# Performance work log

Measured on AMD Instinct MI355X. Metric: run time of the kernel, lower is better.

The kernel has to match this reference:

```python
import jax, jax.numpy as jnp
import numpy as np

B, T, S, H = 32, 512, 1024, 512


def setup_inputs() -> dict:
    key = jax.random.key(0)
    k1, k2, k3, k4, k5, k6 = jax.random.split(key, 6)
    scale = 1.0 / np.sqrt(H)
    return {
        "query": jax.random.normal(k1, (B, T, H), dtype=jnp.float32),
        "encoder_outputs": jax.random.normal(k2, (B, S, H), dtype=jnp.float32),
        "src_lengths": jax.random.randint(k3, (B,), 1, S + 1, dtype=jnp.int32),
        "Ws": jax.random.normal(k4, (H, H), dtype=jnp.float32) * scale,  # torch Linear weight [out,in]
        "Wh": jax.random.normal(k5, (H, H), dtype=jnp.float32) * scale,
        "v": jax.random.normal(k6, (H,), dtype=jnp.float32) * scale,
    }


def reference(query, encoder_outputs, src_lengths, Ws, Wh, v):
    # score(h_s, q_t) = v^T tanh(Wh h_s + Ws q_t); masked softmax over src; weighted sum.
    S_ = encoder_outputs.shape[1]
    # Wh(encoder_outputs) computed once (loop in original recomputes it each step; same math).
    Whe = jnp.einsum('bsh,oh->bso', encoder_outputs, Wh)  # [B,S,H]
    mask = jnp.arange(S_)[None, :] < src_lengths[:, None]  # [B,S] valid positions

    def step(carry, q_t):  # q_t: [B,H]
        Wsq = jnp.einsum('bh,oh->bo', q_t, Ws)            # [B,H]
        scores = jnp.einsum('bsh,h->bs', jnp.tanh(Whe + Wsq[:, None, :]), v)  # [B,S]
        scores = jnp.where(mask, scores, -jnp.inf)
        attn = jax.nn.softmax(scores, axis=-1)            # [B,S]
        ctx = jnp.einsum('bs,bsh->bh', attn, encoder_outputs)  # [B,H]
        return carry, (ctx, attn)

    _, (ctx_t, attn_t) = jax.lax.scan(step, None, jnp.swapaxes(query, 0, 1))
    context_vectors = jnp.swapaxes(ctx_t, 0, 1)  # [B,T,H]
    # original returns attention weights from the LAST timestep only
    return context_vectors, attn_t[-1]
```

## Files before the change

### kernel.cpp

```cpp
#include <hip/hip_runtime.h>


constexpr int B = 32, T = 512, S = 1024, H = 512;
constexpr int TT = 16;
constexpr float C2LOG2E = 2.88539008177792681f;

typedef float vf4 __attribute__((ext_vector_type(4)));
typedef float f32x4 __attribute__((ext_vector_type(4)));
typedef short bf16x8 __attribute__((ext_vector_type(8)));
typedef unsigned short ushort_t;

#define DEVI __device__ __forceinline__

DEVI unsigned pack_bf16(float a, float b) {
  unsigned ua = __builtin_bit_cast(unsigned, a) + 0x8000u;
  unsigned ub = __builtin_bit_cast(unsigned, b) + 0x8000u;
  return (ub & 0xffff0000u) | (ua >> 16);
}
DEVI ushort_t to_bf16u(float x) {
  return (ushort_t)((__builtin_bit_cast(unsigned, x) + 0x8000u) >> 16);
}
DEVI float bf_lo(unsigned d) { return __builtin_bit_cast(float, d << 16); }
DEVI float bf_hi(unsigned d) { return __builtin_bit_cast(float, d & 0xffff0000u); }
DEVI float bf_one(ushort_t u) { return __builtin_bit_cast(float, (unsigned)u << 16); }
DEVI float exp2c(float x) {
  return __builtin_amdgcn_exp2f(fminf(fmaxf(x, -15.f), 15.f));
}

constexpr int QBLK = (B * T / 128) * 4;
constexpr int EBLK = (B * S / 128) * 4;

__global__ __launch_bounds__(256)
void mfma_matmul_kernel(const float* __restrict__ query, const float* __restrict__ enc,
                        const float* __restrict__ Ws, const float* __restrict__ Wh,
                        float* __restrict__ q4, float* __restrict__ e4,
                        const int* __restrict__ lens) {
  __shared__ short As[128][72];
  __shared__ short Bs[128][72];
  const int tid = threadIdx.x;
  int blk = blockIdx.x;
  const bool isE = blk >= QBLK;
  if (isE) blk -= QBLK;
  const int bx = blk & 3, by = blk >> 2;
  const int row0 = by * 128, col0 = bx * 128;
  const float* A = isE ? enc : query;
  const float* W = isE ? Wh : Ws;
  if (isE && (row0 % S) >= lens[row0 / S]) return;

  const int lr = tid >> 4;
  const int lc = (tid & 15) * 4;
  const int lane = tid & 63, wv = tid >> 6;
  const int wm = (wv >> 1) * 64, wn = (wv & 1) * 64;
  const int lrow = lane & 15, lkg = (lane >> 4) * 8;

  f32x4 acc[4][4] = {};
  for (int k0 = 0; k0 < H; k0 += 64) {
    __syncthreads();
#pragma unroll
    for (int u = 0; u < 8; ++u) {
      int r = lr + u * 16;
      float4 av = *(const float4*)&A[(size_t)(row0 + r) * H + k0 + lc];
      *(uint2*)&As[r][lc] = make_uint2(pack_bf16(av.x, av.y), pack_bf16(av.z, av.w));
      float4 wv4 = *(const float4*)&W[(size_t)(col0 + r) * H + k0 + lc];
      *(uint2*)&Bs[r][lc] = make_uint2(pack_bf16(wv4.x, wv4.y), pack_bf16(wv4.z, wv4.w));
    }
    __syncthreads();
#pragma unroll
    for (int ks = 0; ks < 64; ks += 32) {
      bf16x8 af[4], bfr[4];
#pragma unroll
      for (int i = 0; i < 4; ++i) {
        af[i] = *(const bf16x8*)&As[wm + i * 16 + lrow][ks + lkg];
        bfr[i] = *(const bf16x8*)&Bs[wn + i * 16 + lrow][ks + lkg];
      }
#pragma unroll
      for (int mt = 0; mt < 4; ++mt)
#pragma unroll
        for (int nt = 0; nt < 4; ++nt)
          acc[mt][nt] = __builtin_amdgcn_mfma_f32_16x16x32_bf16(
              af[mt], bfr[nt], acc[mt][nt], 0, 0, 0);
    }
  }

  const int crow = (lane >> 4) * 4, ccol = lane & 15;
  if (!isE) {
    const int b = row0 / T;
#pragma unroll
    for (int mt = 0; mt < 4; ++mt) {
      const int m = (row0 % T) + wm + mt * 16 + crow;
      const int tile_t = m >> 2;
#pragma unroll
      for (int nt = 0; nt < 4; ++nt) {
        const int n = col0 + wn + nt * 16 + ccol;
        float* base = q4 + (size_t)b * T * H + (size_t)tile_t * (4 * H) +
                      (n >> 2) * 16 + (n & 3);
        f32x4 a = acc[mt][nt];
#pragma unroll
        for (int reg = 0; reg < 4; ++reg) base[reg * 4] = exp2c(C2LOG2E * a[reg]);
      }
    }
  } else {
    const int b = row0 / S;
#pragma unroll
    for (int mt = 0; mt < 4; ++mt) {
      const int s0 = (row0 % S) + wm + mt * 16 + crow;
#pragma unroll
      for (int nt = 0; nt < 4; ++nt) {
        const int n = col0 + wn + nt * 16 + ccol;
        float* base = e4 + (size_t)b * H * S + (size_t)(n >> 2) * (4 * S) +
                      (size_t)s0 * 4 + (n & 3);
        f32x4 a = acc[mt][nt];
#pragma unroll
        for (int reg = 0; reg < 4; ++reg) base[reg * 4] = exp2c(C2LOG2E * a[reg]);
      }
    }
  }
}

DEVI void tree4(float& acc, vf4 q, vf4 vv, vf4 e) {
  float a0 = __builtin_fmaf(q[0], e[0], 1.0f);
  float a1 = __builtin_fmaf(q[1], e[1], 1.0f);
  float a2 = __builtin_fmaf(q[2], e[2], 1.0f);
  float a3 = __builtin_fmaf(q[3], e[3], 1.0f);
  float d01 = a0 * a1, d23 = a2 * a3;
  float n01 = __builtin_fmaf(vv[1], a0, vv[0] * a1);
  float n23 = __builtin_fmaf(vv[3], a2, vv[2] * a3);
  float d = d01 * d23;
  float n = __builtin_fmaf(n23, d01, n01 * d23);
  acc = __builtin_fmaf(n, __builtin_amdgcn_rcpf(d), acc);
}

DEVI vf4 qload4(const ushort_t (&s_q4)[32][64], int h4q, int t) {
  uint2 qu = *(const uint2*)&s_q4[h4q][t * 4];
  vf4 q = {bf_lo(qu.x), bf_hi(qu.x), bf_lo(qu.y), bf_hi(qu.y)};
  return q;
}

DEVI void stage_quarter(ushort_t (&s_q4)[32][64], const vf4* __restrict__ qsrc,
                        int qt, int tid) {
  __syncthreads();
#pragma unroll
  for (int u = 0; u < 2; ++u) {
    int g = tid + u * 256;
    int tile = g >> 7, rem = g & 127;
    int h4q = rem >> 2, i = rem & 3;
    vf4 qv = qsrc[tile * 512 + (qt * 32 + h4q) * 4 + i];
    uint2 pk = make_uint2(pack_bf16(qv[0], qv[1]), pack_bf16(qv[2], qv[3]));
    ((uint2*)&s_q4[0][0])[h4q * 16 + tile * 4 + i] = pk;
  }
  __syncthreads();
}

template <int NSIM>
DEVI void passN16(ushort_t (&s_q4)[32][64], const vf4* __restrict__ qsrc,
                  const float* __restrict__ v, const float* __restrict__ e4b,
                  ushort_t (&s_sc16)[TT][S], int wv, int lane) {
  const int tid = wv * 64 + lane;
  float acc[NSIM][TT];
#pragma unroll
  for (int r = 0; r < NSIM; ++r)
#pragma unroll
    for (int t = 0; t < TT; ++t) acc[r][t] = 0.f;
  const float* ep = e4b + (size_t)(wv * 64 + lane) * 4;
  for (int qt = 0; qt < 4; ++qt) {
    stage_quarter(s_q4, qsrc, qt, tid);
    for (int h4q = 0; h4q < 32; ++h4q) {
      const int h4 = qt * 32 + h4q;
      vf4 e[NSIM];
#pragma unroll
      for (int r = 0; r < NSIM; ++r)
        e[r] = *(const vf4*)(ep + (size_t)h4 * (S * 4) + r * 1024);
      vf4 vv = *(const vf4*)(v + h4 * 4);
#pragma unroll
      for (int t = 0; t < TT; ++t) {
        vf4 q = qload4(s_q4, h4q, t);
#pragma unroll
        for (int r = 0; r < NSIM; ++r) tree4(acc[r][t], q, vv, e[r]);
      }
    }
  }
#pragma unroll
  for (int r = 0; r < NSIM; ++r) {
    const int s = (wv + 4 * r) * 64 + lane;
#pragma unroll
    for (int t = 0; t < TT; ++t) s_sc16[t][s] = to_bf16u(-2.0f * acc[r][t]);
  }
}

template <int R>
DEVI void passTail16(ushort_t (&s_q4)[32][64], const vf4* __restrict__ qsrc,
                     const float* __restrict__ v, const float* __restrict__ e4b,
                     ushort_t (&s_sc16)[TT][S], int kbase, int wv, int lane) {
  const int tid = wv * 64 + lane;
  float acc[R][4];
#pragma unroll
  for (int r = 0; r < R; ++r)
#pragma unroll
    for (int jj = 0; jj < 4; ++jj) acc[r][jj] = 0.f;
  const float* ep = e4b + (size_t)(kbase * 64 + lane) * 4;
  for (int qt = 0; qt < 4; ++qt) {
    stage_quarter(s_q4, qsrc, qt, tid);
    for (int h4q = 0; h4q < 32; ++h4q) {
      const int h4 = qt * 32 + h4q;
      vf4 vv = *(const vf4*)(v + h4 * 4);
      vf4 e[R];
#pragma unroll
      for (int r = 0; r < R; ++r)
        e[r] = *(const vf4*)(ep + (size_t)h4 * (S * 4) + r * 256);
#pragma unroll
      for (int jj = 0; jj < 4; ++jj) {
        vf4 q = qload4(s_q4, h4q, wv + 4 * jj);
#pragma unroll
        for (int r = 0; r < R; ++r) tree4(acc[r][jj], q, vv, e[r]);
      }
    }
  }
#pragma unroll
  for (int r = 0; r < R; ++r)
#pragma unroll
    for (int jj = 0; jj < 4; ++jj)
      s_sc16[wv + 4 * jj][(kbase + r) * 64 + lane] = to_bf16u(-2.0f * acc[r][jj]);
}

__global__ __launch_bounds__(256, 4)
void attn_fused_kernel(const float* __restrict__ wsq, const float* __restrict__ wheT,
                       const float* __restrict__ enc, const float* __restrict__ v,
                       const int* __restrict__ lens, float* __restrict__ out) {
  __shared__ __align__(16) ushort_t s_sc16[TT][S];
  __shared__ __align__(16) ushort_t s_q4[32][64];
  __shared__ float s_rs[TT];
  __shared__ long long s_w[32];
  __shared__ int s_bsel;

  const int tid = threadIdx.x;
  const int xcd = blockIdx.x & 7;
  const int j = blockIdx.x >> 3;
  const int slot = j >> 5;
  const int tt = j & 31;

  if (tid < 32) s_w[tid] = ((long long)lens[tid] << 8) + tid;
  __syncthreads();
  if (tid < 32) {
    long long wb = s_w[tid];
    int rank = 0;
#pragma unroll
    for (int b2 = 0; b2 < 32; ++b2) rank += (s_w[b2] > wb);
    int myrank = slot * 8 + ((slot & 1) ? (7 - xcd) : xcd);
    if (rank == myrank) s_bsel = tid;
  }
  __syncthreads();
  const int b = __builtin_amdgcn_readfirstlane(s_bsel);
  const int len = lens[b];

  {
    const int wv = tid >> 6, lane = tid & 63;
    const int NS = (len + 63) >> 6;
    const int nsw = NS >> 2;
    const int R = NS & 3;
    const float* e4b = wheT + (size_t)b * H * S;
    const vf4* qsrc = (const vf4*)(wsq + (size_t)b * T * H + (size_t)tt * (TT * H));
    switch (nsw) {
      case 1: passN16<1>(s_q4, qsrc, v, e4b, s_sc16, wv, lane); break;
      case 2: passN16<2>(s_q4, qsrc, v, e4b, s_sc16, wv, lane); break;
      case 3: passN16<3>(s_q4, qsrc, v, e4b, s_sc16, wv, lane); break;
      case 4: passN16<4>(s_q4, qsrc, v, e4b, s_sc16, wv, lane); break;
      default: break;
    }
    switch (R) {
      case 1: passTail16<1>(s_q4, qsrc, v, e4b, s_sc16, nsw * 4, wv, lane); break;
      case 2: passTail16<2>(s_q4, qsrc, v, e4b, s_sc16, nsw * 4, wv, lane); break;
      case 3: passTail16<3>(s_q4, qsrc, v, e4b, s_sc16, nsw * 4, wv, lane); break;
      default: break;
    }
  }
  __syncthreads();

  {
    const int wv = tid >> 6, lane = tid & 63;
#pragma unroll
    for (int jj = 0; jj < 4; ++jj) {
      const int tr = wv + 4 * jj;
      float vals[S / 64], ps[S / 64];
      float m = -3.0e38f;
#pragma unroll
      for (int i = 0; i < S / 64; ++i) {
        int s = lane + 64 * i;
        vals[i] = bf_one(s_sc16[tr][s]);
        if (s < len) m = fmaxf(m, vals[i]);
      }
#pragma unroll
      for (int o = 1; o < 64; o <<= 1) m = fmaxf(m, __shfl_xor(m, o, 64));
      float sum = 0.f;
#pragma unroll
      for (int i = 0; i < S / 64; ++i) {
        int s = lane + 64 * i;
        float p = (s < len) ? __builtin_amdgcn_exp2f((vals[i] - m) * 1.44269504088896341f) : 0.f;
        ps[i] = p;
        sum += p;
      }
#pragma unroll
      for (int o = 1; o < 64; o <<= 1) sum += __shfl_xor(sum, o, 64);
      float rs = 1.0f / sum;
#pragma unroll
      for (int i = 0; i < S / 64; ++i) s_sc16[tr][lane + 64 * i] = to_bf16u(ps[i]);
      if (lane == 0) s_rs[tr] = rs;
      if (tt == T / TT - 1 && tr == TT - 1) {
#pragma unroll
        for (int i = 0; i < S / 64; ++i)
          out[(size_t)B * T * H + (size_t)b * S + lane + 64 * i] = ps[i] * rs;
      }
    }
  }
  __syncthreads();

  {
    const int wv = tid >> 6, lane = tid & 63;
    const int h0 = lane * 4, h1 = 256 + lane * 4;
    float acc[4][8] = {};
    const float* encb = enc + (size_t)b * S * H;
    const int len4 = (len + 3) & ~3;
    for (int s0 = 0; s0 < len4; s0 += 4) {
      vf4 pr[4];
#pragma unroll
      for (int jj = 0; jj < 4; ++jj) {
        uint2 pu = *(const uint2*)&s_sc16[wv + 4 * jj][s0];
        pr[jj] = (vf4){bf_lo(pu.x), bf_hi(pu.x), bf_lo(pu.y), bf_hi(pu.y)};
      }
#pragma unroll
      for (int kk = 0; kk < 4; ++kk) {
        const float* er = encb + (size_t)(s0 + kk) * H;
        float4 e0 = *(const float4*)(er + h0);
        float4 e1 = *(const float4*)(er + h1);
        float ev[8] = {e0.x, e0.y, e0.z, e0.w, e1.x, e1.y, e1.z, e1.w};
#pragma unroll
        for (int jj = 0; jj < 4; ++jj)
#pragma unroll
          for (int q = 0; q < 8; ++q)
            acc[jj][q] = __builtin_fmaf(pr[jj][kk], ev[q], acc[jj][q]);
      }
    }
#pragma unroll
    for (int jj = 0; jj < 4; ++jj) {
      const int tr = wv + 4 * jj;
      const float rs = s_rs[tr];
      const size_t base = ((size_t)b * T + tt * TT + tr) * H;
      float4 o;
      o = make_float4(acc[jj][0] * rs, acc[jj][1] * rs, acc[jj][2] * rs, acc[jj][3] * rs);
      *(float4*)&out[base + h0] = o;
      o = make_float4(acc[jj][4] * rs, acc[jj][5] * rs, acc[jj][6] * rs, acc[jj][7] * rs);
      *(float4*)&out[base + h1] = o;
    }
  }
}

extern "C" void kernel_launch(void* const* d_in, const int* in_sizes, int n_in,
                              void* d_out, int out_size, void* d_ws, size_t ws_size,
                              hipStream_t stream) {
  const float* query = (const float*)d_in[0];
  const float* enc   = (const float*)d_in[1];
  const int*   lens  = (const int*)d_in[2];
  const float* Ws    = (const float*)d_in[3];
  const float* Wh    = (const float*)d_in[4];
  const float* v     = (const float*)d_in[5];
  float* out = (float*)d_out;
  float* wsq  = (float*)d_ws;
  float* wheT = wsq + (size_t)B * T * H;

  mfma_matmul_kernel<<<dim3(QBLK + EBLK), 256, 0, stream>>>(query, enc, Ws, Wh, wsq, wheT, lens);
  attn_fused_kernel<<<dim3(B * (T / TT)), 256, 0, stream>>>(wsq, wheT, enc, v, lens, out);
}
```

Measured before the change: 560.5 us.

## Compute context accumulation with bf16 MFMA and drop softmax max pass

The context-vector stage is rewritten from per-thread scalar FMAs over float4 encoder rows to bf16 16x16x32 MFMA instructions. Attention probabilities are now taken straight from LDS, and encoder values are converted to bf16 on the fly. Softmax skips the max-reduction pass because tanh-bounded scores cannot overflow exp, and it normalizes probabilities before storing them. The score LDS buffer rows are padded to reduce bank conflicts. In exchange, encoder values lose precision in bf16, and the encoder loads become strided scalar reads instead of wide vector loads.

```diff
diff --git a/kernel.cpp b/kernel.cpp
--- a/kernel.cpp
+++ b/kernel.cpp
@@ -3,6 +3,7 @@
 
 constexpr int B = 32, T = 512, S = 1024, H = 512;
 constexpr int TT = 16;
+constexpr int SP = S + 8;
 constexpr float C2LOG2E = 2.88539008177792681f;
 
 typedef float vf4 __attribute__((ext_vector_type(4)));
@@ -154,7 +155,7 @@
 template <int NSIM>
 DEVI void passN16(ushort_t (&s_q4)[32][64], const vf4* __restrict__ qsrc,
                   const float* __restrict__ v, const float* __restrict__ e4b,
-                  ushort_t (&s_sc16)[TT][S], int wv, int lane) {
+                  ushort_t (&s_sc16)[TT][SP], int wv, int lane) {
   const int tid = wv * 64 + lane;
   float acc[NSIM][TT];
 #pragma unroll
@@ -190,7 +191,7 @@
 template <int R>
 DEVI void passTail16(ushort_t (&s_q4)[32][64], const vf4* __restrict__ qsrc,
                      const float* __restrict__ v, const float* __restrict__ e4b,
-                     ushort_t (&s_sc16)[TT][S], int kbase, int wv, int lane) {
+                     ushort_t (&s_sc16)[TT][SP], int kbase, int wv, int lane) {
   const int tid = wv * 64 + lane;
   float acc[R][4];
 #pragma unroll
@@ -226,9 +227,8 @@
 void attn_fused_kernel(const float* __restrict__ wsq, const float* __restrict__ wheT,
                        const float* __restrict__ enc, const float* __restrict__ v,
                        const int* __restrict__ lens, float* __restrict__ out) {
-  __shared__ __align__(16) ushort_t s_sc16[TT][S];
+  __shared__ __align__(16) ushort_t s_sc16[TT][SP];
   __shared__ __align__(16) ushort_t s_q4[32][64];
-  __shared__ float s_rs[TT];
   __shared__ long long s_w[32];
   __shared__ int s_bsel;
 
@@ -280,21 +280,13 @@
 #pragma unroll
     for (int jj = 0; jj < 4; ++jj) {
       const int tr = wv + 4 * jj;
-      float vals[S / 64], ps[S / 64];
-      float m = -3.0e38f;
+      float ps[S / 64];
+      float sum = 0.f;
 #pragma unroll
       for (int i = 0; i < S / 64; ++i) {
         int s = lane + 64 * i;
-        vals[i] = bf_one(s_sc16[tr][s]);
-        if (s < len) m = fmaxf(m, vals[i]);
-      }
-#pragma unroll
-      for (int o = 1; o < 64; o <<= 1) m = fmaxf(m, __shfl_xor(m, o, 64));
-      float sum = 0.f;
-#pragma unroll
-      for (int i = 0; i < S / 64; ++i) {
-        int s = lane + 64 * i;
-        float p = (s < len) ? __builtin_amdgcn_exp2f((vals[i] - m) * 1.44269504088896341f) : 0.f;
+        float sc = bf_one(s_sc16[tr][s]);
+        float p = (s < len) ? __builtin_amdgcn_exp2f(sc * 1.44269504088896341f) : 0.f;
         ps[i] = p;
         sum += p;
       }
@@ -302,12 +294,11 @@
       for (int o = 1; o < 64; o <<= 1) sum += __shfl_xor(sum, o, 64);
       float rs = 1.0f / sum;
 #pragma unroll
-      for (int i = 0; i < S / 64; ++i) s_sc16[tr][lane + 64 * i] = to_bf16u(ps[i]);
-      if (lane == 0) s_rs[tr] = rs;
-      if (tt == T / TT - 1 && tr == TT - 1) {
-#pragma unroll
-        for (int i = 0; i < S / 64; ++i)
-          out[(size_t)B * T * H + (size_t)b * S + lane + 64 * i] = ps[i] * rs;
+      for (int i = 0; i < S / 64; ++i) {
+        float pn = ps[i] * rs;
+        s_sc16[tr][lane + 64 * i] = to_bf16u(pn);
+        if (tt == T / TT - 1 && tr == TT - 1)
+          out[(size_t)B * T * H + (size_t)b * S + lane + 64 * i] = pn;
       }
     }
   }
@@ -315,40 +306,35 @@
 
   {
     const int wv = tid >> 6, lane = tid & 63;
-    const int h0 = lane * 4, h1 = 256 + lane * 4;
-    float acc[4][8] = {};
+    const int lrow = lane & 15, lkg = (lane >> 4) * 8;
+    const int hbase = wv * 128;
     const float* encb = enc + (size_t)b * S * H;
-    const int len4 = (len + 3) & ~3;
-    for (int s0 = 0; s0 < len4; s0 += 4) {
-      vf4 pr[4];
-#pragma unroll
-      for (int jj = 0; jj < 4; ++jj) {
-        uint2 pu = *(const uint2*)&s_sc16[wv + 4 * jj][s0];
-        pr[jj] = (vf4){bf_lo(pu.x), bf_hi(pu.x), bf_lo(pu.y), bf_hi(pu.y)};
-      }
-#pragma unroll
-      for (int kk = 0; kk < 4; ++kk) {
-        const float* er = encb + (size_t)(s0 + kk) * H;
-        float4 e0 = *(const float4*)(er + h0);
-        float4 e1 = *(const float4*)(er + h1);
-        float ev[8] = {e0.x, e0.y, e0.z, e0.w, e1.x, e1.y, e1.z, e1.w};
-#pragma unroll
-        for (int jj = 0; jj < 4; ++jj)
-#pragma unroll
-          for (int q = 0; q < 8; ++q)
-            acc[jj][q] = __builtin_fmaf(pr[jj][kk], ev[q], acc[jj][q]);
-      }
-    }
-#pragma unroll
-    for (int jj = 0; jj < 4; ++jj) {
-      const int tr = wv + 4 * jj;
-      const float rs = s_rs[tr];
-      const size_t base = ((size_t)b * T + tt * TT + tr) * H;
-      float4 o;
-      o = make_float4(acc[jj][0] * rs, acc[jj][1] * rs, acc[jj][2] * rs, acc[jj][3] * rs);
-      *(float4*)&out[base + h0] = o;
-      o = make_float4(acc[jj][4] * rs, acc[jj][5] * rs, acc[jj][6] * rs, acc[jj][7] * rs);
-      *(float4*)&out[base + h1] = o;
+    f32x4 acc[8] = {};
+    const int nch = (len + 31) >> 5;
+    for (int kc = 0; kc < nch; ++kc) {
+      const int k0 = kc * 32 + lkg;
+      bf16x8 pa = *(const bf16x8*)&s_sc16[lrow][k0];
+#pragma unroll
+      for (int nt = 0; nt < 8; ++nt) {
+        const int h = hbase + nt * 16 + lrow;
+        const float* ep = encb + (size_t)k0 * H + h;
+        float b0 = ep[0 * H], b1 = ep[1 * H], b2 = ep[2 * H], b3 = ep[3 * H];
+        float b4 = ep[4 * H], b5 = ep[5 * H], b6 = ep[6 * H], b7 = ep[7 * H];
+        uint4 uu = make_uint4(pack_bf16(b0, b1), pack_bf16(b2, b3),
+                              pack_bf16(b4, b5), pack_bf16(b6, b7));
+        bf16x8 bfr = __builtin_bit_cast(bf16x8, uu);
+        acc[nt] = __builtin_amdgcn_mfma_f32_16x16x32_bf16(pa, bfr, acc[nt], 0, 0, 0);
+      }
+    }
+    const int crow = (lane >> 4) * 4, ccol = lane & 15;
+#pragma unroll
+    for (int nt = 0; nt < 8; ++nt) {
+      const int h = hbase + nt * 16 + ccol;
+#pragma unroll
+      for (int reg = 0; reg < 4; ++reg) {
+        const int t = crow + reg;
+        out[((size_t)b * T + tt * TT + t) * H + h] = acc[nt][reg];
+      }
     }
   }
 }
```

Result: faster. 496.2 us, median of 2 (-11.5%).
